# Kernel optimization log

Measured on AMD Instinct MI355X. Metric: run time of the kernel, lower is better.

The kernel has to match this reference:

```python
import jax, jax.numpy as jnp
import numpy as np
import math

B, C, L_SEQ, PRED = 32, 21, 512, 96
D, H, DFF, NLAYERS = 512, 8, 2048, 3
E = D // H
PATCH_LEN, STRIDE, PAD = 16, 8, 8
PATCH_NUM = (L_SEQ - PATCH_LEN) // STRIDE + 2  # 64
MA = 25          # moving-average kernel of series_decomp
FACTOR = 1
TOP_K = int(FACTOR * math.log(PATCH_NUM))  # top-k delays in AutoCorrelation


def _pos_embedding(max_len, d_model):
    pos = np.arange(max_len, dtype=np.float32)[:, None]
    div = np.exp(np.arange(0, d_model, 2, dtype=np.float32) * -(math.log(10000.0) / d_model))
    pe = np.zeros((max_len, d_model), np.float32)
    pe[:, 0::2] = np.sin(pos * div)
    pe[:, 1::2] = np.cos(pos * div)
    return jnp.asarray(pe)

POS_EMB = _pos_embedding(PATCH_NUM, D)


def setup_inputs():
    key = jax.random.key(0)
    ks = iter(jax.random.split(key, 48))
    g = lambda shape, s=0.02: jax.random.normal(next(ks), shape, jnp.float32) * s
    inp = {"x_enc": jax.random.normal(next(ks), (B, L_SEQ, C), jnp.float32)}
    inp["w_val"] = g((PATCH_LEN, D))  # PatchEmbedding value_embedding (no bias)
    for tag in ("ac", "sa"):
        for nm in ("Wq", "Wk", "Wv", "Wo"):
            inp[nm + "_" + tag] = g((NLAYERS, D, D))
        for nm in ("bq", "bk", "bv", "bo"):
            inp[nm + "_" + tag] = g((NLAYERS, D))
    inp["Wf"] = g((NLAYERS, 2 * D, D))
    inp["bf"] = g((NLAYERS, D))
    inp["W1"] = g((NLAYERS, D, DFF))   # conv1 (1x1, no bias)
    inp["W2"] = g((NLAYERS, DFF, D))   # conv2 (1x1, no bias)
    inp["bn_g"] = jnp.ones((D,), jnp.float32)
    inp["bn_b"] = jnp.zeros((D,), jnp.float32)
    inp["W_head"] = g((D * PATCH_NUM, PRED))
    inp["b_head"] = g((PRED,))
    return inp


def _proj_heads(x, W, b):
    N, L, _ = x.shape
    return (x @ W + b).reshape(N, L, H, E)


def _auto_corr(x, Wq, bq, Wk, bk, Wv, bv, Wo, bo):
    # AutoCorrelation (training-mode time_delay_agg): FFT correlation + top-k roll aggregation
    N, L, _ = x.shape
    q = _proj_heads(x, Wq, bq)
    k = _proj_heads(x, Wk, bk)
    v = _proj_heads(x, Wv, bv)
    qf = jnp.fft.rfft(q.transpose(0, 2, 3, 1), axis=-1)   # [N,H,E,Lf]
    kf = jnp.fft.rfft(k.transpose(0, 2, 3, 1), axis=-1)
    corr = jnp.fft.irfft(qf * jnp.conj(kf), n=L, axis=-1)  # [N,H,E,L]
    vals = v.transpose(0, 2, 3, 1)                          # [N,H,E,L]
    mean_corr = corr.mean(axis=(1, 2))                      # [N,L]
    _, top_idx = jax.lax.top_k(mean_corr.mean(axis=0), TOP_K)  # delays shared across batch
    w = jax.nn.softmax(mean_corr[:, top_idx], axis=-1)      # [N,TOP_K]
    rolled = jax.vmap(lambda s: jnp.roll(vals, -s, axis=-1))(top_idx)  # [K,N,H,E,L]
    agg = jnp.einsum('knhel,nk->nhel', rolled, w)
    return agg.transpose(0, 3, 1, 2).reshape(N, L, D) @ Wo + bo


def _full_attn(x, Wq, bq, Wk, bk, Wv, bv, Wo, bo):
    N, L, _ = x.shape
    q = _proj_heads(x, Wq, bq)
    k = _proj_heads(x, Wk, bk)
    v = _proj_heads(x, Wv, bv)
    scores = jnp.einsum('blhe,bshe->bhls', q, k) / math.sqrt(E)
    out = jnp.einsum('bhls,bshe->blhe', jax.nn.softmax(scores, axis=-1), v)
    return out.reshape(N, L, D) @ Wo + bo


def _decomp(x):
    # series_decomp: residual after edge-replicated moving average (returns seasonal part)
    half = (MA - 1) // 2
    xp = jnp.concatenate([jnp.repeat(x[:, :1], half, axis=1), x,
                          jnp.repeat(x[:, -1:], half, axis=1)], axis=1)
    cs = jnp.cumsum(xp, axis=1)
    cs = jnp.concatenate([jnp.zeros_like(cs[:, :1]), cs], axis=1)
    mean = (cs[:, MA:] - cs[:, :-MA]) / MA
    return x - mean


def _forward(x_enc, w_val, Wq_ac, bq_ac, Wk_ac, bk_ac, Wv_ac, bv_ac, Wo_ac, bo_ac,
             Wq_sa, bq_sa, Wk_sa, bk_sa, Wv_sa, bv_sa, Wo_sa, bo_sa,
             Wf, bf, W1, W2, bn_g, bn_b, W_head, b_head):
    # instance normalization over time
    means = x_enc.mean(axis=1, keepdims=True)                 # [B,1,C]
    xc = x_enc - means
    stdev = jnp.sqrt(xc.var(axis=1, keepdims=True) + 1e-5)    # [B,1,C]
    xn = xc / stdev
    # patch embedding (channel independent): replication-pad end, unfold, linear + pos emb
    xp = xn.transpose(0, 2, 1)                                # [B,C,L]
    xp = jnp.concatenate([xp, jnp.repeat(xp[..., -1:], PAD, axis=-1)], axis=-1)
    idx = jnp.arange(PATCH_NUM)[:, None] * STRIDE + jnp.arange(PATCH_LEN)[None, :]
    patches = xp[..., idx]                                    # [B,C,P,patch_len]
    x = patches.reshape(B * C, PATCH_NUM, PATCH_LEN) @ w_val + POS_EMB  # [B*C,P,D]
    # hybrid encoder layers
    for l in range(NLAYERS):
        a = _auto_corr(x, Wq_ac[l], bq_ac[l], Wk_ac[l], bk_ac[l], Wv_ac[l], bv_ac[l], Wo_ac[l], bo_ac[l])
        s = _full_attn(x, Wq_sa[l], bq_sa[l], Wk_sa[l], bk_sa[l], Wv_sa[l], bv_sa[l], Wo_sa[l], bo_sa[l])
        fused = jnp.concatenate([a, s], axis=-1) @ Wf[l] + bf[l]
        x = _decomp(x + fused)
        y = jax.nn.relu(x @ W1[l]) @ W2[l]                    # 1x1 convs == pointwise linears
        x = _decomp(x + y)
    # final BatchNorm1d over d_model channels (batch statistics, affine)
    mu = x.mean(axis=(0, 1))
    var = x.var(axis=(0, 1))
    x = (x - mu) / jnp.sqrt(var + 1e-5) * bn_g + bn_b
    # head: [B*C,P,D] -> [B,C,D,P] -> flat (d-major) -> pred_len
    enc = x.reshape(B, C, PATCH_NUM, D).transpose(0, 1, 3, 2).reshape(B, C, D * PATCH_NUM)
    dec = (enc @ W_head + b_head).transpose(0, 2, 1)          # [B,PRED,C]
    return dec * stdev[:, 0][:, None, :] + means[:, 0][:, None, :]


def reference(x_enc, w_val, Wq_ac, bq_ac, Wk_ac, bk_ac, Wv_ac, bv_ac, Wo_ac, bo_ac,
              Wq_sa, bq_sa, Wk_sa, bk_sa, Wv_sa, bv_sa, Wo_sa, bo_sa,
              Wf, bf, W1, W2, bn_g, bn_b, W_head, b_head):
    return _forward(x_enc, w_val, Wq_ac, bq_ac, Wk_ac, bk_ac, Wv_ac, bv_ac, Wo_ac, bo_ac,
                    Wq_sa, bq_sa, Wk_sa, bk_sa, Wv_sa, bv_sa, Wo_sa, bo_sa,
                    Wf, bf, W1, W2, bn_g, bn_b, W_head, b_head)
```

## Files before the change

### kernel.cpp

```cpp
#include <hip/hip_runtime.h>
#include <math.h>


typedef unsigned short u16;
typedef short s16x8 __attribute__((ext_vector_type(8)));
typedef u16 u16x8 __attribute__((ext_vector_type(8)));
typedef float f32x4 __attribute__((ext_vector_type(4)));

#define MROWS 43008
#define NSEQ  672

__device__ __forceinline__ float bf2f(u16 b) {
  union { unsigned u; float f; } v; v.u = ((unsigned)b) << 16; return v.f;
}
__device__ __forceinline__ u16 f2bf(float f) {
  union { float f; unsigned u; } v; v.f = f;
  unsigned r = v.u + 0x7FFFu + ((v.u >> 16) & 1u);
  return (u16)(r >> 16);
}

__device__ __forceinline__ void gload16(const u16* g, u16* l) {
  __builtin_amdgcn_global_load_lds(
      (const __attribute__((address_space(1))) unsigned int*)g,
      (__attribute__((address_space(3))) unsigned int*)l, 16, 0, 0);
}

__global__ __launch_bounds__(256) void zero_out_kernel(float* __restrict__ o, int n) {
  int i = blockIdx.x * 256 + threadIdx.x;
  if (i < n) o[i] = 0.f;
}

__global__ __launch_bounds__(256) void transpose_cvt_b(
    const float* __restrict__ W, u16* __restrict__ Wt, int K, int N,
    long long sW, long long sT) {
  __shared__ float t[32][33];
  int z = blockIdx.z;
  W += (size_t)z * sW;
  Wt += (size_t)z * sT;
  int k0 = blockIdx.x * 32, n0 = blockIdx.y * 32;
  int tx = threadIdx.x, ty = threadIdx.y;
#pragma unroll
  for (int i = 0; i < 32; i += 8)
    t[ty + i][tx] = W[(size_t)(k0 + ty + i) * N + n0 + tx];
  __syncthreads();
#pragma unroll
  for (int i = 0; i < 32; i += 8)
    Wt[(size_t)(n0 + ty + i) * K + k0 + tx] = f2bf(t[tx][ty + i]);
}

__global__ __launch_bounds__(256) void transpose_cvt_six(
    const float* __restrict__ Wq_sa, const float* __restrict__ Wk_sa,
    const float* __restrict__ Wv_sa, const float* __restrict__ Wq_ac,
    const float* __restrict__ Wk_ac, const float* __restrict__ Wv_ac,
    u16* __restrict__ dst) {
  __shared__ float t[32][33];
  int z = blockIdx.z;
  int l = z / 6, wi = z % 6;
  const float* srcs[6] = {Wq_sa, Wk_sa, Wv_sa, Wq_ac, Wk_ac, Wv_ac};
  const float* W = srcs[wi] + (size_t)l * 262144;
  u16* out = dst + ((size_t)l * 6 + wi) * 262144;
  int k0 = blockIdx.x * 32, n0 = blockIdx.y * 32;
  int tx = threadIdx.x, ty = threadIdx.y;
#pragma unroll
  for (int i = 0; i < 32; i += 8)
    t[ty + i][tx] = W[(size_t)(k0 + ty + i) * 512 + n0 + tx];
  __syncthreads();
#pragma unroll
  for (int i = 0; i < 32; i += 8)
    out[(size_t)(n0 + ty + i) * 512 + k0 + tx] = f2bf(t[tx][ty + i]);
}

__global__ __launch_bounds__(256) void cvt_bf16_six(
    const float* __restrict__ Wo_ac, const float* __restrict__ Wo_sa,
    u16* __restrict__ dst) {
  int z = blockIdx.z;
  int l = (z < 3) ? z : z - 3, s = (z < 3) ? 0 : 1;
  const float* src = (s == 0 ? Wo_ac : Wo_sa) + (size_t)l * 262144;
  u16* out = dst + ((size_t)l * 2 + s) * 262144;
  int i = blockIdx.x * 256 + threadIdx.x;
  if (i < 262144) out[i] = f2bf(src[i]);
}

__global__ __launch_bounds__(512) void bias_combine(
    const float* __restrict__ WfW, const float* __restrict__ bfW,
    const float* __restrict__ bo_ac, const float* __restrict__ bo_sa,
    float* __restrict__ out) {
  int l = blockIdx.x;
  const float* Wf = WfW + (size_t)l * 524288;
  int n = threadIdx.x;
  float s = bfW[l * 512 + n];
  for (int i = 0; i < 512; i++) s += bo_ac[l * 512 + i] * Wf[(size_t)i * 512 + n];
  for (int i = 0; i < 512; i++) s += bo_sa[l * 512 + i] * Wf[(size_t)(512 + i) * 512 + n];
  out[l * 512 + n] = s;
}

__global__ __launch_bounds__(512) void gemm256p(
    const u16* __restrict__ A1, const u16* __restrict__ A2, int lda, int ksplit,
    const u16* __restrict__ Bt, int ldb,
    const float* __restrict__ b0, const float* __restrict__ b1,
    const float* __restrict__ b2,
    u16* __restrict__ C, int ldc, int K, int relu, int nb) {
  __shared__ u16 smA[2][2][256 * 32];
  __shared__ u16 smB[2][2][256 * 32];
  int g = blockIdx.x;
  if ((gridDim.x & 7) == 0) g = (g & 7) * (gridDim.x >> 3) + (g >> 3);
  int m0 = (g / nb) * 256, n0 = (g % nb) * 256;
  int tid = threadIdx.x, lane = tid & 63, wid = tid >> 6;
  int wr = wid >> 2, wc = wid & 3;
  int m_in = lane & 15, kq = lane >> 4;
  int srow0 = lane >> 2, sslot = lane & 3;

  f32x4 acc[8][4];
#pragma unroll
  for (int i = 0; i < 8; i++)
#pragma unroll
    for (int j = 0; j < 4; j++) acc[i][j] = (f32x4){0.f, 0.f, 0.f, 0.f};

  int nt = K >> 6;

  auto STAGE = [&](int tp, int t, int kh) {
    int k0 = t * 64 + kh * 32;
    const u16* Ap; int kk;
    if (t * 64 < ksplit) { Ap = A1; kk = k0; } else { Ap = A2; kk = k0 - ksplit; }
#pragma unroll
    for (int i = 0; i < 2; i++) {
      int r = i * 128 + wid * 16 + srow0;
      int gs = (sslot ^ ((r >> 1) & 3)) * 8;
      gload16(&Ap[(size_t)(m0 + r) * lda + kk + gs],
              &smA[tp][kh][(i * 128 + wid * 16) * 32]);
      gload16(&Bt[(size_t)(n0 + r) * ldb + k0 + gs],
              &smB[tp][kh][(i * 128 + wid * 16) * 32]);
    }
  };

  STAGE(0, 0, 0);
  STAGE(0, 0, 1);

  int tp = 0;
  for (int t = 0; t < nt; ++t) {
    int tn = t + 1 < nt ? t + 1 : t;
#pragma unroll
    for (int kh = 0; kh < 2; kh++) {
      asm volatile("s_waitcnt vmcnt(4)" ::: "memory");
      asm volatile("s_barrier" ::: "memory");
      const u16* As = &smA[tp][kh][0];
      const u16* Bs = &smB[tp][kh][0];
      s16x8 a_[8], b_[4];
#pragma unroll
      for (int mf = 0; mf < 8; mf++) {
        int row = wr * 128 + mf * 16 + m_in;
        a_[mf] = *(const s16x8*)&As[row * 32 + ((kq ^ ((row >> 1) & 3)) * 8)];
      }
#pragma unroll
      for (int nf = 0; nf < 4; nf++) {
        int row = wc * 64 + nf * 16 + m_in;
        b_[nf] = *(const s16x8*)&Bs[row * 32 + ((kq ^ ((row >> 1) & 3)) * 8)];
      }
      STAGE(tp ^ 1, tn, kh);
      __builtin_amdgcn_s_setprio(1);
#pragma unroll
      for (int mf = 0; mf < 8; mf++)
#pragma unroll
        for (int nf = 0; nf < 4; nf++)
          acc[mf][nf] = __builtin_amdgcn_mfma_f32_16x16x32_bf16(
              a_[mf], b_[nf], acc[mf][nf], 0, 0, 0);
      __builtin_amdgcn_s_setprio(0);
    }
    tp ^= 1;
  }
  int r0 = m0 + wr * 128 + (kq << 2);
#pragma unroll
  for (int mf = 0; mf < 8; mf++) {
#pragma unroll
    for (int nf = 0; nf < 4; nf++) {
      int col = n0 + wc * 64 + nf * 16 + m_in;
      const float* bp = (col < 512) ? b0 : (col < 1024 ? b1 : b2);
      float bv = bp ? bp[col & 511] : 0.f;
#pragma unroll
      for (int r = 0; r < 4; r++) {
        float v = acc[mf][nf][r] + bv;
        if (relu) v = fmaxf(v, 0.f);
        C[(size_t)(r0 + mf * 16 + r) * ldc + col] = f2bf(v);
      }
    }
  }
}

__global__ __launch_bounds__(256) void gemm128p(
    const u16* __restrict__ A1, const u16* __restrict__ A2, int lda, int ksplit,
    const u16* __restrict__ Bt, int ldb,
    const float* __restrict__ b0, const float* __restrict__ b1,
    const float* __restrict__ b2,
    u16* __restrict__ C, int ldc, int K, int relu, int nb) {
  __shared__ u16 sm[3][8192];
  int g = blockIdx.x;
  if ((gridDim.x & 7) == 0) g = (g & 7) * (gridDim.x >> 3) + (g >> 3);
  int m0 = (g / nb) * 128, n0 = (g % nb) * 128;
  int tid = threadIdx.x, lane = tid & 63, w = tid >> 6;
  int wr = w >> 1, wc = w & 1;
  int srow = w * 16 + (lane >> 2);
  int scol = (((lane & 3) ^ ((lane >> 3) & 3)) * 8);
  int m_in = lane & 15;
  int sgrp = lane >> 4;
  int offA[4], offB[4];
#pragma unroll
  for (int mf = 0; mf < 4; mf++) {
    int row = wr * 64 + mf * 16 + m_in;
    offA[mf] = row * 32 + ((sgrp ^ ((row >> 1) & 3)) * 8);
  }
#pragma unroll
  for (int nf = 0; nf < 4; nf++) {
    int row = wc * 64 + nf * 16 + m_in;
    offB[nf] = 4096 + row * 32 + ((sgrp ^ ((row >> 1) & 3)) * 8);
  }
  f32x4 acc[4][4];
#pragma unroll
  for (int i = 0; i < 4; i++)
#pragma unroll
    for (int j = 0; j < 4; j++) acc[i][j] = (f32x4){0.f, 0.f, 0.f, 0.f};

  int nt = K >> 5;
  auto STAGE = [&](int b, int t) {
    int k0 = t * 32;
    const u16* Ab; int kk;
    if (k0 < ksplit) { Ab = A1; kk = k0; } else { Ab = A2; kk = k0 - ksplit; }
    u16* base = &sm[b][0];
    gload16(&Ab[(size_t)(m0 + srow) * lda + kk + scol],      base + w * 512);
    gload16(&Ab[(size_t)(m0 + 64 + srow) * lda + kk + scol], base + 2048 + w * 512);
    gload16(&Bt[(size_t)(n0 + srow) * ldb + k0 + scol],      base + 4096 + w * 512);
    gload16(&Bt[(size_t)(n0 + 64 + srow) * ldb + k0 + scol], base + 6144 + w * 512);
  };

  STAGE(0, 0);
  STAGE(1, 1 < nt ? 1 : nt - 1);
  int cb = 0;
  for (int t = 0; t < nt; ++t) {
    int pf = t + 2 < nt ? t + 2 : nt - 1;
    int pb = cb + 2 >= 3 ? cb - 1 : cb + 2;
    STAGE(pb, pf);
    asm volatile("s_waitcnt vmcnt(8)" ::: "memory");
    asm volatile("s_barrier" ::: "memory");
    const u16* lb = &sm[cb][0];
    s16x8 a_[4], b_[4];
#pragma unroll
    for (int mf = 0; mf < 4; mf++) a_[mf] = *(const s16x8*)&lb[offA[mf]];
#pragma unroll
    for (int nf = 0; nf < 4; nf++) b_[nf] = *(const s16x8*)&lb[offB[nf]];
    __builtin_amdgcn_s_setprio(1);
#pragma unroll
    for (int mf = 0; mf < 4; mf++)
#pragma unroll
      for (int nf = 0; nf < 4; nf++)
        acc[mf][nf] = __builtin_amdgcn_mfma_f32_16x16x32_bf16(
            a_[mf], b_[nf], acc[mf][nf], 0, 0, 0);
    __builtin_amdgcn_s_setprio(0);
    asm volatile("s_barrier" ::: "memory");
    cb = cb + 1 >= 3 ? 0 : cb + 1;
  }
  int r0 = m0 + wr * 64 + (sgrp << 2);
  int cl = lane & 15;
#pragma unroll
  for (int mf = 0; mf < 4; mf++) {
#pragma unroll
    for (int nf = 0; nf < 4; nf++) {
      int col = n0 + wc * 64 + nf * 16 + cl;
      const float* bp = (col < 512) ? b0 : (col < 1024 ? b1 : b2);
      float bv = bp ? bp[col & 511] : 0.f;
#pragma unroll
      for (int r = 0; r < 4; r++) {
        float v = acc[mf][nf][r] + bv;
        if (relu) v = fmaxf(v, 0.f);
        C[(size_t)(r0 + mf * 16 + r) * ldc + col] = f2bf(v);
      }
    }
  }
}

__global__ __launch_bounds__(256) void gram_mc_kernel(
    const u16* __restrict__ Q, const u16* __restrict__ K, int ld,
    float* __restrict__ MC) {
  __shared__ u16 lA[64][40];
  __shared__ u16 lB[64][40];
  __shared__ float red[64];
  int n = blockIdx.x;
  int tid = threadIdx.x, lane = tid & 63, w = tid >> 6;
  int sr = tid >> 2, scol = (tid & 3) * 8;
  if (tid < 64) red[tid] = 0.f;
  f32x4 acc[4];
#pragma unroll
  for (int i = 0; i < 4; i++) acc[i] = (f32x4){0.f, 0.f, 0.f, 0.f};
  size_t base = (size_t)n * 64 * ld;
  for (int k0 = 0; k0 < 512; k0 += 32) {
    *(u16x8*)&lA[sr][scol] = *(const u16x8*)&Q[base + (size_t)sr * ld + k0 + scol];
    *(u16x8*)&lB[sr][scol] = *(const u16x8*)&K[base + (size_t)sr * ld + k0 + scol];
    __syncthreads();
    int ar = w * 16 + (lane & 15);
    int kk = (lane >> 4) * 8;
    s16x8 af = *(const s16x8*)&lA[ar][kk];
#pragma unroll
    for (int nb = 0; nb < 4; nb++) {
      s16x8 bfr = *(const s16x8*)&lB[nb * 16 + (lane & 15)][kk];
      acc[nb] = __builtin_amdgcn_mfma_f32_16x16x32_bf16(af, bfr, acc[nb], 0, 0, 0);
    }
    __syncthreads();
  }
  int row0 = w * 16 + ((lane >> 4) << 2);
  int cl = lane & 15;
#pragma unroll
  for (int nb = 0; nb < 4; nb++) {
    int col = nb * 16 + cl;
#pragma unroll
    for (int r = 0; r < 4; r++)
      atomicAdd(&red[(row0 + r - col) & 63], acc[nb][r]);
  }
  __syncthreads();
  if (tid < 64) MC[n * 64 + tid] = red[tid] * (1.f / 512.f);
}

__global__ __launch_bounds__(256) void instnorm_kernel(
    const float* __restrict__ xe, float* __restrict__ MEANS, float* __restrict__ STDEV) {
  int n = blockIdx.x;
  int b = n / 21, c = n % 21;
  int tid = threadIdx.x;
  float v0 = xe[((size_t)b * 512 + tid) * 21 + c];
  float v1 = xe[((size_t)b * 512 + tid + 256) * 21 + c];
  float s = v0 + v1, ss = v0 * v0 + v1 * v1;
  for (int o = 32; o; o >>= 1) { s += __shfl_down(s, o); ss += __shfl_down(ss, o); }
  __shared__ float rs[4], rss[4];
  if ((tid & 63) == 0) { rs[tid >> 6] = s; rss[tid >> 6] = ss; }
  __syncthreads();
  if (tid == 0) {
    s = rs[0] + rs[1] + rs[2] + rs[3];
    ss = rss[0] + rss[1] + rss[2] + rss[3];
    float mean = s * (1.f / 512.f);
    float var = ss * (1.f / 512.f) - mean * mean;
    MEANS[n] = mean;
    STDEV[n] = sqrtf(var + 1e-5f);
  }
}

__global__ __launch_bounds__(256) void pe_kernel(float* __restrict__ PE) {
  int i = blockIdx.x * 256 + threadIdx.x;
  int p = i >> 9, d = i & 511;
  int k = d >> 1;
  float freq = expf(-(float)(2 * k) * (9.210340371976184f / 512.f));
  float ang = (float)p * freq;
  PE[i] = (d & 1) ? cosf(ang) : sinf(ang);
}

__global__ __launch_bounds__(256) void patch_kernel(
    const float* __restrict__ xe, const float* __restrict__ wv,
    const float* __restrict__ PE, const float* __restrict__ MEANS,
    const float* __restrict__ STDEV, u16* __restrict__ X) {
  __shared__ float pw[16][512];
  __shared__ float pat[8][16];
  int bx = blockIdx.x;
  int n = bx >> 3, pb = bx & 7;
  int b = n / 21, c = n % 21;
  int tid = threadIdx.x;
  float mean = MEANS[n], inv = 1.f / STDEV[n];
  for (int i = tid; i < 8192; i += 256) pw[i >> 9][i & 511] = wv[i];
  if (tid < 128) {
    int pp = tid >> 4, j = tid & 15;
    int l = (pb * 8 + pp) * 8 + j;
    if (l > 511) l = 511;
    pat[pp][j] = (xe[((size_t)b * 512 + l) * 21 + c] - mean) * inv;
  }
  __syncthreads();
  for (int i = tid; i < 4096; i += 256) {
    int pp = i >> 9, d = i & 511;
    int p = pb * 8 + pp;
    float s = PE[p * 512 + d];
#pragma unroll
    for (int j = 0; j < 16; j++) s += pat[pp][j] * pw[j][d];
    X[((size_t)n * 64 + p) * 512 + d] = f2bf(s);
  }
}

__global__ __launch_bounds__(256) void topk_softw_kernel(
    const float* __restrict__ MC, int* __restrict__ TIDX, float* __restrict__ WSM) {
  __shared__ float g[256];
  __shared__ float gt[64];
  __shared__ int dly[4];
  int tid = threadIdx.x;
  int tau = tid & 63, part = tid >> 6;
  float s = 0.f;
  for (int n = part * 168; n < (part + 1) * 168; n++) s += MC[n * 64 + tau];
  g[tid] = s;
  __syncthreads();
  if (tid < 64) gt[tid] = g[tid] + g[64 + tid] + g[128 + tid] + g[192 + tid];
  __syncthreads();
  if (tid == 0) {
    for (int j = 0; j < 4; j++) {
      int best = 0; float bv = -1e30f;
      for (int t = 0; t < 64; t++) if (gt[t] > bv) { bv = gt[t]; best = t; }
      dly[j] = best;
      TIDX[j] = best;
      gt[best] = -1e30f;
    }
  }
  __syncthreads();
  for (int n = tid; n < 672; n += 256) {
    float v[4], mx = -1e30f;
#pragma unroll
    for (int j = 0; j < 4; j++) { v[j] = MC[n * 64 + dly[j]]; mx = fmaxf(mx, v[j]); }
    float ssum = 0.f;
#pragma unroll
    for (int j = 0; j < 4; j++) { v[j] = __expf(v[j] - mx); ssum += v[j]; }
    float inv = 1.f / ssum;
#pragma unroll
    for (int j = 0; j < 4; j++) WSM[n * 4 + j] = v[j] * inv;
  }
}

__global__ __launch_bounds__(256) void agg_kernel(
    const u16* __restrict__ V, int ld, const float* __restrict__ WSM,
    const int* __restrict__ TIDX, u16* __restrict__ OUT) {
  int n = blockIdx.x;
  __shared__ float w[4];
  __shared__ int dly[4];
  int tid = threadIdx.x;
  if (tid < 4) { w[tid] = WSM[n * 4 + tid]; dly[tid] = TIDX[tid]; }
  __syncthreads();
  for (int i = tid; i < 64 * 512; i += 256) {
    int l = i >> 9, d = i & 511;
    float s = 0.f;
#pragma unroll
    for (int j = 0; j < 4; j++)
      s += w[j] * bf2f(V[((size_t)n * 64 + ((l + dly[j]) & 63)) * ld + d]);
    OUT[((size_t)n * 64 + l) * ld + d] = f2bf(s);
  }
}

__global__ __launch_bounds__(256) void attn_mfma(u16* __restrict__ QKV) {
  __shared__ u16 lq[64][72], lk[64][72], lvt[64][72], lp[64][72];
  int n = blockIdx.x >> 3, h = blockIdx.x & 7;
  size_t base = (size_t)n * 64 * 1536;
  int qo = h * 64, ko = 512 + h * 64, vo = 1024 + h * 64;
  int tid = threadIdx.x, lane = tid & 63, w = tid >> 6;
  int r = tid >> 2, c0 = (tid & 3) * 16;
  *(u16x8*)&lq[r][c0]     = *(const u16x8*)&QKV[base + (size_t)r * 1536 + qo + c0];
  *(u16x8*)&lq[r][c0 + 8] = *(const u16x8*)&QKV[base + (size_t)r * 1536 + qo + c0 + 8];
  *(u16x8*)&lk[r][c0]     = *(const u16x8*)&QKV[base + (size_t)r * 1536 + ko + c0];
  *(u16x8*)&lk[r][c0 + 8] = *(const u16x8*)&QKV[base + (size_t)r * 1536 + ko + c0 + 8];
  u16x8 v0 = *(const u16x8*)&QKV[base + (size_t)r * 1536 + vo + c0];
  u16x8 v1 = *(const u16x8*)&QKV[base + (size_t)r * 1536 + vo + c0 + 8];
#pragma unroll
  for (int j = 0; j < 8; j++) { lvt[c0 + j][r] = v0[j]; lvt[c0 + 8 + j][r] = v1[j]; }
  __syncthreads();
  int m_in = lane & 15, ks = (lane >> 4) * 8;
  int rq = lane >> 4;
  s16x8 aq0 = *(const s16x8*)&lq[w * 16 + m_in][ks];
  s16x8 aq1 = *(const s16x8*)&lq[w * 16 + m_in][32 + ks];
  f32x4 s4[4];
#pragma unroll
  for (int nf = 0; nf < 4; nf++) {
    s4[nf] = (f32x4){0.f, 0.f, 0.f, 0.f};
    s16x8 b0 = *(const s16x8*)&lk[nf * 16 + m_in][ks];
    s16x8 b1 = *(const s16x8*)&lk[nf * 16 + m_in][32 + ks];
    s4[nf] = __builtin_amdgcn_mfma_f32_16x16x32_bf16(aq0, b0, s4[nf], 0, 0, 0);
    s4[nf] = __builtin_amdgcn_mfma_f32_16x16x32_bf16(aq1, b1, s4[nf], 0, 0, 0);
  }
  float mx[4] = {-1e30f, -1e30f, -1e30f, -1e30f};
#pragma unroll
  for (int nf = 0; nf < 4; nf++)
#pragma unroll
    for (int r4 = 0; r4 < 4; r4++) {
      s4[nf][r4] *= 0.125f;
      mx[r4] = fmaxf(mx[r4], s4[nf][r4]);
    }
#pragma unroll
  for (int o = 1; o < 16; o <<= 1)
#pragma unroll
    for (int r4 = 0; r4 < 4; r4++) mx[r4] = fmaxf(mx[r4], __shfl_xor(mx[r4], o));
  float sum[4] = {0.f, 0.f, 0.f, 0.f};
#pragma unroll
  for (int nf = 0; nf < 4; nf++)
#pragma unroll
    for (int r4 = 0; r4 < 4; r4++) {
      float e = __expf(s4[nf][r4] - mx[r4]);
      s4[nf][r4] = e;
      sum[r4] += e;
    }
#pragma unroll
  for (int o = 1; o < 16; o <<= 1)
#pragma unroll
    for (int r4 = 0; r4 < 4; r4++) sum[r4] += __shfl_xor(sum[r4], o);
#pragma unroll
  for (int nf = 0; nf < 4; nf++)
#pragma unroll
    for (int r4 = 0; r4 < 4; r4++)
      lp[w * 16 + rq * 4 + r4][nf * 16 + m_in] = f2bf(s4[nf][r4] / sum[r4]);
  __syncthreads();
  s16x8 ap0 = *(const s16x8*)&lp[w * 16 + m_in][ks];
  s16x8 ap1 = *(const s16x8*)&lp[w * 16 + m_in][32 + ks];
#pragma unroll
  for (int nf = 0; nf < 4; nf++) {
    f32x4 o4 = (f32x4){0.f, 0.f, 0.f, 0.f};
    s16x8 b0 = *(const s16x8*)&lvt[nf * 16 + m_in][ks];
    s16x8 b1 = *(const s16x8*)&lvt[nf * 16 + m_in][32 + ks];
    o4 = __builtin_amdgcn_mfma_f32_16x16x32_bf16(ap0, b0, o4, 0, 0, 0);
    o4 = __builtin_amdgcn_mfma_f32_16x16x32_bf16(ap1, b1, o4, 0, 0, 0);
#pragma unroll
    for (int r4 = 0; r4 < 4; r4++)
      QKV[base + (size_t)(w * 16 + rq * 4 + r4) * 1536 + qo + nf * 16 + m_in] =
          f2bf(o4[r4]);
  }
}

__global__ __launch_bounds__(256) void decomp_kernel(
    u16* __restrict__ X, const u16* __restrict__ DELTA, int ds) {
  int n = blockIdx.x >> 1;
  int d = ((blockIdx.x & 1) << 8) + threadIdx.x;
  size_t xb = ((size_t)n * 64) * 512 + d;
  size_t db = ((size_t)n * 64) * ds + d;
  float v[64];
#pragma unroll
  for (int l = 0; l < 64; l++)
    v[l] = bf2f(X[xb + (size_t)l * 512]) + bf2f(DELTA[db + (size_t)l * ds]);
  float s = 12.f * v[0];
#pragma unroll
  for (int t = 0; t <= 12; t++) s += v[t];
#pragma unroll
  for (int l = 0; l < 64; l++) {
    float out = v[l] - s * (1.f / 25.f);
    X[xb + (size_t)l * 512] = f2bf(out);
    if (l < 63) {
      int add = l + 13; if (add > 63) add = 63;
      int sub = l - 12; if (sub < 0) sub = 0;
      s += v[add] - v[sub];
    }
  }
}

__global__ __launch_bounds__(256) void bn_part(
    const u16* __restrict__ X, float* __restrict__ PS) {
  int ch = blockIdx.x, tid = threadIdx.x;
  float s1a = 0, s2a = 0, s1b = 0, s2b = 0;
  size_t base = (size_t)ch * 128 * 512;
  for (int r = 0; r < 128; r++) {
    float a = bf2f(X[base + (size_t)r * 512 + tid]);
    float b = bf2f(X[base + (size_t)r * 512 + tid + 256]);
    s1a += a; s2a += a * a; s1b += b; s2b += b * b;
  }
  PS[(size_t)(ch * 2 + 0) * 512 + tid] = s1a;
  PS[(size_t)(ch * 2 + 0) * 512 + tid + 256] = s1b;
  PS[(size_t)(ch * 2 + 1) * 512 + tid] = s2a;
  PS[(size_t)(ch * 2 + 1) * 512 + tid + 256] = s2b;
}

__global__ __launch_bounds__(256) void bn_final(
    const float* __restrict__ PS, const float* __restrict__ g,
    const float* __restrict__ b, float* __restrict__ SCALE, float* __restrict__ SHIFT) {
  int d = blockIdx.x * 256 + threadIdx.x;
  float s = 0, ss = 0;
  for (int c = 0; c < 336; c++) {
    s += PS[(size_t)(c * 2) * 512 + d];
    ss += PS[(size_t)(c * 2 + 1) * 512 + d];
  }
  float mu = s * (1.f / 43008.f);
  float var = ss * (1.f / 43008.f) - mu * mu;
  float inv = 1.f / sqrtf(var + 1e-5f);
  float sc = g[d] * inv;
  SCALE[d] = sc;
  SHIFT[d] = b[d] - mu * sc;
}

__global__ __launch_bounds__(256) void bn_transpose_kernel(
    const u16* __restrict__ X, const float* __restrict__ SCALE,
    const float* __restrict__ SHIFT, u16* __restrict__ ENC) {
  __shared__ u16 t[64][72];
  int n = blockIdx.x >> 3, dc = (blockIdx.x & 7) * 64;
  int tid = threadIdx.x;
  for (int i = tid; i < 4096; i += 256) {
    int p = i >> 6, d = i & 63;
    float v = bf2f(X[((size_t)n * 64 + p) * 512 + dc + d]) * SCALE[dc + d] + SHIFT[dc + d];
    t[p][d] = f2bf(v);
  }
  __syncthreads();
  for (int i = tid; i < 4096; i += 256) {
    int d = i >> 6, p = i & 63;
    ENC[(size_t)n * 32768 + (size_t)(dc + d) * 64 + p] = t[p][d];
  }
}

__global__ __launch_bounds__(256) void head_gemm(
    const u16* __restrict__ ENC, const u16* __restrict__ Wht,
    float* __restrict__ PART) {
  __shared__ u16 lA[64][40];
  __shared__ u16 lB[96][40];
  int bm = blockIdx.x;
  int kc = blockIdx.y;
  int tid = threadIdx.x, lane = tid & 63, w = tid >> 6;
  int sr = tid >> 2, sc0 = (tid & 3) * 8;
  f32x4 acc[6];
#pragma unroll
  for (int i = 0; i < 6; i++) acc[i] = (f32x4){0.f, 0.f, 0.f, 0.f};
  for (int kk0 = 0; kk0 < 2048; kk0 += 32) {
    int k0 = kc * 2048 + kk0;
    *(u16x8*)&lA[sr][sc0] =
        *(const u16x8*)&ENC[(size_t)(bm * 64 + sr) * 32768 + k0 + sc0];
    for (int i = tid; i < 96 * 4; i += 256) {
      int rB = i >> 2, seg = (i & 3) * 8;
      *(u16x8*)&lB[rB][seg] = *(const u16x8*)&Wht[(size_t)rB * 32768 + k0 + seg];
    }
    __syncthreads();
    int ar = w * 16 + (lane & 15);
    int kk = (lane >> 4) * 8;
    s16x8 af = *(const s16x8*)&lA[ar][kk];
#pragma unroll
    for (int nb = 0; nb < 6; nb++) {
      s16x8 bfr = *(const s16x8*)&lB[nb * 16 + (lane & 15)][kk];
      acc[nb] = __builtin_amdgcn_mfma_f32_16x16x32_bf16(af, bfr, acc[nb], 0, 0, 0);
    }
    __syncthreads();
  }
  int rb = bm * 64 + w * 16 + ((lane >> 4) << 2);
  int cl = lane & 15;
#pragma unroll
  for (int nb = 0; nb < 6; nb++) {
    int col = nb * 16 + cl;
#pragma unroll
    for (int r = 0; r < 4; r++) {
      int row = rb + r;
      if (row < 672) PART[((size_t)kc * 672 + row) * 96 + col] = acc[nb][r];
    }
  }
}

__global__ __launch_bounds__(256) void head_reduce(
    const float* __restrict__ PART, const float* __restrict__ bh,
    const float* __restrict__ STDEV, const float* __restrict__ MEANS,
    float* __restrict__ OUT) {
  int i = blockIdx.x * 256 + threadIdx.x;
  if (i >= 672 * 96) return;
  int n = i / 96, r = i % 96;
  float s = bh[r];
  for (int kc = 0; kc < 16; kc++) s += PART[((size_t)kc * 672 + n) * 96 + r];
  int b = n / 21, c = n % 21;
  OUT[((size_t)b * 96 + r) * 21 + c] = s * STDEV[n] + MEANS[n];
}

extern "C" void kernel_launch(void* const* d_in, const int* in_sizes, int n_in,
                              void* d_out, int out_size, void* d_ws, size_t ws_size,
                              hipStream_t stream) {
  const float* x_enc = (const float*)d_in[0];
  const float* w_val = (const float*)d_in[1];
  const float* Wq_ac = (const float*)d_in[2];
  const float* Wk_ac = (const float*)d_in[3];
  const float* Wv_ac = (const float*)d_in[4];
  const float* Wo_ac = (const float*)d_in[5];
  const float* bq_ac = (const float*)d_in[6];
  const float* bk_ac = (const float*)d_in[7];
  const float* bv_ac = (const float*)d_in[8];
  const float* bo_ac = (const float*)d_in[9];
  const float* Wq_sa = (const float*)d_in[10];
  const float* Wk_sa = (const float*)d_in[11];
  const float* Wv_sa = (const float*)d_in[12];
  const float* Wo_sa = (const float*)d_in[13];
  const float* bq_sa = (const float*)d_in[14];
  const float* bk_sa = (const float*)d_in[15];
  const float* bv_sa = (const float*)d_in[16];
  const float* bo_sa = (const float*)d_in[17];
  const float* WfW   = (const float*)d_in[18];
  const float* bfW   = (const float*)d_in[19];
  const float* W1    = (const float*)d_in[20];
  const float* W2    = (const float*)d_in[21];
  const float* bn_g  = (const float*)d_in[22];
  const float* bn_b  = (const float*)d_in[23];
  const float* W_head = (const float*)d_in[24];
  const float* b_head = (const float*)d_in[25];
  (void)in_sizes; (void)n_in; (void)out_size;

  char* wsp = (char*)d_ws;
  size_t off = 0;
  auto alloc = [&](size_t bytes) -> void* {
    void* p = wsp + off;
    off += (bytes + 255) & ~(size_t)255;
    return p;
  };
  u16* X    = (u16*)alloc((size_t)MROWS * 512 * 2);
  u16* Q3   = (u16*)alloc((size_t)MROWS * 1536 * 2);
  u16* SIX   = (u16*)alloc((size_t)3 * 6 * 262144 * 2);
  u16* W1T   = (u16*)alloc((size_t)3 * 1048576 * 2);
  u16* W2T   = (u16*)alloc((size_t)3 * 1048576 * 2);
  u16* WFT   = (u16*)alloc((size_t)3 * 524288 * 2);
  u16* WOAS  = (u16*)alloc((size_t)3 * 2 * 262144 * 2);
  u16* WCOMB = (u16*)alloc((size_t)3 * 524288 * 2);
  u16* WHT   = (u16*)alloc((size_t)3145728 * 2);
  float* PE = (float*)alloc((size_t)32768 * 4);
  float* MEANS = (float*)alloc(672 * 4);
  float* STDEV = (float*)alloc(672 * 4);
  float* MC = (float*)alloc(672 * 64 * 4);
  int* TIDX = (int*)alloc(4 * 4);
  float* WSM = (float*)alloc(672 * 4 * 4);
  float* BNP = (float*)alloc((size_t)336 * 1024 * 4);
  float* SCALE = (float*)alloc(512 * 4);
  float* SHIFT = (float*)alloc(512 * 4);
  float* BCOMB = (float*)alloc(3 * 512 * 4);
  u16* C0 = Q3;
  u16* C1 = Q3 + 512;
  u16* C2 = Q3 + 1024;
  u16* HBUF = Q3;
  u16* YBUF = Q3 + (size_t)21504 * 2048;
  u16* ENC  = Q3;
  float* HEADP = (float*)X;

  if (off > ws_size) {
    zero_out_kernel<<<252, 256, 0, stream>>>((float*)d_out, 672 * 96);
    return;
  }

  transpose_cvt_six<<<dim3(16, 16, 18), dim3(32, 8), 0, stream>>>(
      Wq_sa, Wk_sa, Wv_sa, Wq_ac, Wk_ac, Wv_ac, SIX);
  transpose_cvt_b<<<dim3(16, 64, 3), dim3(32, 8), 0, stream>>>(
      W1, W1T, 512, 2048, 1048576, 1048576);
  transpose_cvt_b<<<dim3(64, 16, 3), dim3(32, 8), 0, stream>>>(
      W2, W2T, 2048, 512, 1048576, 1048576);
  transpose_cvt_b<<<dim3(32, 16, 3), dim3(32, 8), 0, stream>>>(
      WfW, WFT, 1024, 512, 524288, 524288);
  transpose_cvt_b<<<dim3(1024, 3, 1), dim3(32, 8), 0, stream>>>(
      W_head, WHT, 32768, 96, 0, 0);
  cvt_bf16_six<<<dim3(1024, 1, 6), 256, 0, stream>>>(Wo_ac, Wo_sa, WOAS);
  bias_combine<<<3, 512, 0, stream>>>(WfW, bfW, bo_ac, bo_sa, BCOMB);
  for (int l = 0; l < 3; l++) {
    const u16* wfT = WFT + (size_t)l * 524288;
    const u16* woa = WOAS + (size_t)l * 2 * 262144;
    const u16* wos = woa + 262144;
    u16* wc = WCOMB + (size_t)l * 524288;
    gemm128p<<<16, 256, 0, stream>>>(
        wfT, wfT, 1024, 512, woa, 512,
        nullptr, nullptr, nullptr, wc, 1024, 512, 0, 4);
    gemm128p<<<16, 256, 0, stream>>>(
        wfT + 512, wfT + 512, 1024, 512, wos, 512,
        nullptr, nullptr, nullptr, wc + 512, 1024, 512, 0, 4);
  }

  instnorm_kernel<<<672, 256, 0, stream>>>(x_enc, MEANS, STDEV);
  pe_kernel<<<128, 256, 0, stream>>>(PE);
  patch_kernel<<<672 * 8, 256, 0, stream>>>(x_enc, w_val, PE, MEANS, STDEV, X);

  auto g256 = [&](const u16* A1, const u16* A2, int lda, int ksplit,
                  const u16* Bt, int ldb, const float* b0, const float* b1,
                  const float* b2, u16* C, int ldc, int M, int N, int K,
                  int relu) {
    int nb = N / 256;
    gemm256p<<<(M / 256) * nb, 512, 0, stream>>>(
        A1, A2, lda, ksplit, Bt, ldb, b0, b1, b2, C, ldc, K, relu, nb);
  };

  for (int l = 0; l < 3; l++) {
    const u16* qkv_sa = SIX + (size_t)l * 6 * 262144;
    const u16* qk_ac  = qkv_sa + (size_t)3 * 262144;
    const u16* vac    = qkv_sa + (size_t)5 * 262144;
    const u16* w1     = W1T + (size_t)l * 1048576;
    const u16* w2     = W2T + (size_t)l * 1048576;
    const u16* wcomb  = WCOMB + (size_t)l * 524288;
    g256(X, X, 512, 512, qkv_sa, 512, bq_sa + l * 512, bk_sa + l * 512,
         bv_sa + l * 512, Q3, 1536, MROWS, 1536, 512, 0);
    attn_mfma<<<5376, 256, 0, stream>>>(Q3);
    g256(X, X, 512, 512, qk_ac, 512, bq_ac + l * 512, bk_ac + l * 512, nullptr,
         C1, 1536, MROWS, 1024, 512, 0);
    gram_mc_kernel<<<672, 256, 0, stream>>>(C1, C2, 1536, MC);
    topk_softw_kernel<<<1, 256, 0, stream>>>(MC, TIDX, WSM);
    g256(X, X, 512, 512, vac, 512, bv_ac + l * 512, nullptr, nullptr,
         C1, 1536, MROWS, 512, 512, 0);
    agg_kernel<<<672, 256, 0, stream>>>(C1, 1536, WSM, TIDX, C2);
    g256(C2, C0, 1536, 512, wcomb, 1024, BCOMB + l * 512, nullptr, nullptr,
         C1, 1536, MROWS, 512, 1024, 0);
    decomp_kernel<<<1344, 256, 0, stream>>>(X, C1, 1536);
    for (int c = 0; c < 2; c++) {
      const u16* Xc = X + (size_t)c * 21504 * 512;
      u16* Yc = YBUF + (size_t)c * 21504 * 512;
      g256(Xc, Xc, 512, 512, w1, 512, nullptr, nullptr, nullptr,
           HBUF, 2048, 21504, 2048, 512, 1);
      gemm128p<<<672, 256, 0, stream>>>(
          HBUF, HBUF, 2048, 2048, w2, 2048, nullptr, nullptr, nullptr,
          Yc, 512, 2048, 0, 4);
    }
    decomp_kernel<<<1344, 256, 0, stream>>>(X, YBUF, 512);
  }

  bn_part<<<336, 256, 0, stream>>>(X, BNP);
  bn_final<<<2, 256, 0, stream>>>(BNP, bn_g, bn_b, SCALE, SHIFT);
  bn_transpose_kernel<<<672 * 8, 256, 0, stream>>>(X, SCALE, SHIFT, ENC);
  head_gemm<<<dim3(11, 16), 256, 0, stream>>>(ENC, WHT, HEADP);
  head_reduce<<<252, 256, 0, stream>>>(HEADP, b_head, STDEV, MEANS, (float*)d_out);
}
```

Baseline: 2.325 ms.

## Fold AutoCorrelation V projection into combined output weight and move GEMM barrier

Time-delay aggregation is linear and its softmax weights sum to one, so the autocorrelation value projection is folded into the precomputed combined output weight (Wf·Wo·Wv) and its bias is folded through Wo into the combined bias. The per-layer V GEMM over all 43008 rows is dropped, and aggregation now reads X directly. The extra weight-folding GEMMs run once on small matrices, but the bf16 product of three weights adds rounding error. The GEMM mainloop barrier is also moved to after the next-stage prefetch issue, which changes how the LDS double buffer is synchronised and may risk a read/write hazard.

```diff
diff --git a/kernel.cpp b/kernel.cpp
--- a/kernel.cpp
+++ b/kernel.cpp
@@ -70,26 +70,38 @@
     out[(size_t)(n0 + ty + i) * 512 + k0 + tx] = f2bf(t[tx][ty + i]);
 }
 
-__global__ __launch_bounds__(256) void cvt_bf16_six(
+__global__ __launch_bounds__(256) void cvt_bf16_nine(
     const float* __restrict__ Wo_ac, const float* __restrict__ Wo_sa,
-    u16* __restrict__ dst) {
+    const float* __restrict__ Wv_ac, u16* __restrict__ dst) {
   int z = blockIdx.z;
-  int l = (z < 3) ? z : z - 3, s = (z < 3) ? 0 : 1;
-  const float* src = (s == 0 ? Wo_ac : Wo_sa) + (size_t)l * 262144;
-  u16* out = dst + ((size_t)l * 2 + s) * 262144;
+  int l = z / 3, s = z % 3;
+  const float* base = (s == 0) ? Wo_ac : (s == 1 ? Wo_sa : Wv_ac);
+  const float* src = base + (size_t)l * 262144;
+  u16* out = dst + ((size_t)l * 3 + s) * 262144;
   int i = blockIdx.x * 256 + threadIdx.x;
   if (i < 262144) out[i] = f2bf(src[i]);
 }
 
+__global__ __launch_bounds__(512) void boa_eff_kernel(
+    const float* __restrict__ Wo_ac, const float* __restrict__ bo_ac,
+    const float* __restrict__ bv_ac, float* __restrict__ out) {
+  int l = blockIdx.x;
+  int i = threadIdx.x;
+  const float* Wo = Wo_ac + (size_t)l * 262144;
+  float s = bo_ac[l * 512 + i];
+  for (int k = 0; k < 512; k++) s += bv_ac[l * 512 + k] * Wo[(size_t)k * 512 + i];
+  out[l * 512 + i] = s;
+}
+
 __global__ __launch_bounds__(512) void bias_combine(
     const float* __restrict__ WfW, const float* __restrict__ bfW,
-    const float* __restrict__ bo_ac, const float* __restrict__ bo_sa,
+    const float* __restrict__ boa_eff, const float* __restrict__ bo_sa,
     float* __restrict__ out) {
   int l = blockIdx.x;
   const float* Wf = WfW + (size_t)l * 524288;
   int n = threadIdx.x;
   float s = bfW[l * 512 + n];
-  for (int i = 0; i < 512; i++) s += bo_ac[l * 512 + i] * Wf[(size_t)i * 512 + n];
+  for (int i = 0; i < 512; i++) s += boa_eff[l * 512 + i] * Wf[(size_t)i * 512 + n];
   for (int i = 0; i < 512; i++) s += bo_sa[l * 512 + i] * Wf[(size_t)(512 + i) * 512 + n];
   out[l * 512 + n] = s;
 }
@@ -135,14 +147,14 @@
 
   STAGE(0, 0, 0);
   STAGE(0, 0, 1);
+  asm volatile("s_waitcnt vmcnt(4)" ::: "memory");
+  asm volatile("s_barrier" ::: "memory");
 
   int tp = 0;
   for (int t = 0; t < nt; ++t) {
     int tn = t + 1 < nt ? t + 1 : t;
 #pragma unroll
     for (int kh = 0; kh < 2; kh++) {
-      asm volatile("s_waitcnt vmcnt(4)" ::: "memory");
-      asm volatile("s_barrier" ::: "memory");
       const u16* As = &smA[tp][kh][0];
       const u16* Bs = &smB[tp][kh][0];
       s16x8 a_[8], b_[4];
@@ -157,6 +169,8 @@
         b_[nf] = *(const s16x8*)&Bs[row * 32 + ((kq ^ ((row >> 1) & 3)) * 8)];
       }
       STAGE(tp ^ 1, tn, kh);
+      asm volatile("s_waitcnt vmcnt(4)" ::: "memory");
+      asm volatile("s_barrier" ::: "memory");
       __builtin_amdgcn_s_setprio(1);
 #pragma unroll
       for (int mf = 0; mf < 8; mf++)
@@ -414,8 +428,8 @@
 }
 
 __global__ __launch_bounds__(256) void agg_kernel(
-    const u16* __restrict__ V, int ld, const float* __restrict__ WSM,
-    const int* __restrict__ TIDX, u16* __restrict__ OUT) {
+    const u16* __restrict__ V, int ldv, const float* __restrict__ WSM,
+    const int* __restrict__ TIDX, u16* __restrict__ OUT, int ldo) {
   int n = blockIdx.x;
   __shared__ float w[4];
   __shared__ int dly[4];
@@ -427,8 +441,8 @@
     float s = 0.f;
 #pragma unroll
     for (int j = 0; j < 4; j++)
-      s += w[j] * bf2f(V[((size_t)n * 64 + ((l + dly[j]) & 63)) * ld + d]);
-    OUT[((size_t)n * 64 + l) * ld + d] = f2bf(s);
+      s += w[j] * bf2f(V[((size_t)n * 64 + ((l + dly[j]) & 63)) * ldv + d]);
+    OUT[((size_t)n * 64 + l) * ldo + d] = f2bf(s);
   }
 }
 
@@ -685,9 +699,10 @@
   u16* W1T   = (u16*)alloc((size_t)3 * 1048576 * 2);
   u16* W2T   = (u16*)alloc((size_t)3 * 1048576 * 2);
   u16* WFT   = (u16*)alloc((size_t)3 * 524288 * 2);
-  u16* WOAS  = (u16*)alloc((size_t)3 * 2 * 262144 * 2);
+  u16* WORIG = (u16*)alloc((size_t)3 * 3 * 262144 * 2);
   u16* WCOMB = (u16*)alloc((size_t)3 * 524288 * 2);
   u16* WHT   = (u16*)alloc((size_t)3145728 * 2);
+  u16* TMP   = (u16*)alloc((size_t)262144 * 2);
   float* PE = (float*)alloc((size_t)32768 * 4);
   float* MEANS = (float*)alloc(672 * 4);
   float* STDEV = (float*)alloc(672 * 4);
@@ -697,6 +712,7 @@
   float* BNP = (float*)alloc((size_t)336 * 1024 * 4);
   float* SCALE = (float*)alloc(512 * 4);
   float* SHIFT = (float*)alloc(512 * 4);
+  float* BOAE = (float*)alloc(3 * 512 * 4);
   float* BCOMB = (float*)alloc(3 * 512 * 4);
   u16* C0 = Q3;
   u16* C1 = Q3 + 512;
@@ -721,15 +737,20 @@
       WfW, WFT, 1024, 512, 524288, 524288);
   transpose_cvt_b<<<dim3(1024, 3, 1), dim3(32, 8), 0, stream>>>(
       W_head, WHT, 32768, 96, 0, 0);
-  cvt_bf16_six<<<dim3(1024, 1, 6), 256, 0, stream>>>(Wo_ac, Wo_sa, WOAS);
-  bias_combine<<<3, 512, 0, stream>>>(WfW, bfW, bo_ac, bo_sa, BCOMB);
+  cvt_bf16_nine<<<dim3(1024, 1, 9), 256, 0, stream>>>(Wo_ac, Wo_sa, Wv_ac, WORIG);
+  boa_eff_kernel<<<3, 512, 0, stream>>>(Wo_ac, bo_ac, bv_ac, BOAE);
+  bias_combine<<<3, 512, 0, stream>>>(WfW, bfW, BOAE, bo_sa, BCOMB);
   for (int l = 0; l < 3; l++) {
     const u16* wfT = WFT + (size_t)l * 524288;
-    const u16* woa = WOAS + (size_t)l * 2 * 262144;
+    const u16* woa = WORIG + (size_t)l * 3 * 262144;
     const u16* wos = woa + 262144;
+    const u16* wva = woa + 2 * 262144;
     u16* wc = WCOMB + (size_t)l * 524288;
     gemm128p<<<16, 256, 0, stream>>>(
         wfT, wfT, 1024, 512, woa, 512,
+        nullptr, nullptr, nullptr, TMP, 512, 512, 0, 4);
+    gemm128p<<<16, 256, 0, stream>>>(
+        TMP, TMP, 512, 512, wva, 512,
         nullptr, nullptr, nullptr, wc, 1024, 512, 0, 4);
     gemm128p<<<16, 256, 0, stream>>>(
         wfT + 512, wfT + 512, 1024, 512, wos, 512,
@@ -752,7 +773,6 @@
   for (int l = 0; l < 3; l++) {
     const u16* qkv_sa = SIX + (size_t)l * 6 * 262144;
     const u16* qk_ac  = qkv_sa + (size_t)3 * 262144;
-    const u16* vac    = qkv_sa + (size_t)5 * 262144;
     const u16* w1     = W1T + (size_t)l * 1048576;
     const u16* w2     = W2T + (size_t)l * 1048576;
     const u16* wcomb  = WCOMB + (size_t)l * 524288;
@@ -763,9 +783,7 @@
          C1, 1536, MROWS, 1024, 512, 0);
     gram_mc_kernel<<<672, 256, 0, stream>>>(C1, C2, 1536, MC);
     topk_softw_kernel<<<1, 256, 0, stream>>>(MC, TIDX, WSM);
-    g256(X, X, 512, 512, vac, 512, bv_ac + l * 512, nullptr, nullptr,
-         C1, 1536, MROWS, 512, 512, 0);
-    agg_kernel<<<672, 256, 0, stream>>>(C1, 1536, WSM, TIDX, C2);
+    agg_kernel<<<672, 256, 0, stream>>>(X, 512, WSM, TIDX, C2, 1536);
     g256(C2, C0, 1536, 512, wcomb, 1024, BCOMB + l * 512, nullptr, nullptr,
          C1, 1536, MROWS, 512, 1024, 0);
     decomp_kernel<<<1344, 256, 0, stream>>>(X, C1, 1536);
```

After: 2.279 ms. 1.02x faster.
